# Optimization experiments

Hardware: AMD Instinct MI355X
Metric: run time of the kernel (lower is better)

## Reference

```python
import jax, jax.numpy as jnp
import numpy as np

L, B, T, D, H, M = 2, 4, 1024, 256, 4, 1024
EPS = 1e-5  # hk.LayerNorm default


def setup_inputs() -> dict:
    key = jax.random.key(0)
    ks = jax.random.split(key, 12)
    s_in = (2.0 / D) ** 0.5       # VarianceScaling(2.0), fan_in = D
    s_o = (2.0 / (H * D)) ** 0.5  # fan_in = H*D for final projection
    s_m = (1.0 / M) ** 0.5
    g = lambda k, shape, s: jax.random.normal(k, shape, jnp.float32) * s
    return {
        "queries": g(ks[0], (B, T, D), 1.0),
        "Wq": g(ks[1], (L, D, H * D), s_in),
        "bq": jnp.zeros((L, H * D), jnp.float32),
        "Wk": g(ks[2], (L, D, H * D), s_in),
        "bk": jnp.zeros((L, H * D), jnp.float32),
        "Wv": g(ks[3], (L, D, H * D), s_in),
        "bv": jnp.zeros((L, H * D), jnp.float32),
        "Wo": g(ks[4], (L, H * D, D), s_o),
        "bo": jnp.zeros((L, D), jnp.float32),
        "ln1_s": jnp.ones((L, D), jnp.float32),
        "ln1_b": jnp.zeros((L, D), jnp.float32),
        "W1": g(ks[5], (L, D, M), s_in),
        "b1": jnp.zeros((L, M), jnp.float32),
        "W2": g(ks[6], (L, M, D), s_m),
        "b2": jnp.zeros((L, D), jnp.float32),
        "ln2_s": jnp.ones((L, D), jnp.float32),
        "ln2_b": jnp.zeros((L, D), jnp.float32),
    }


def _layernorm(x, s, o):
    m = jnp.mean(x, axis=-1, keepdims=True)
    v = jnp.var(x, axis=-1, keepdims=True)
    return (x - m) * jax.lax.rsqrt(v + EPS) * s + o


def _block(x, Wq, bq, Wk, bk, Wv, bv, Wo, bo, ln1_s, ln1_b, W1, b1, W2, b2, ln2_s, ln2_b):
    # Multi-head self-attention with per-head dim = D (key_size == qkv_size)
    q = (x @ Wq + bq).reshape(B, T, H, D)
    k = (x @ Wk + bk).reshape(B, T, H, D)
    v = (x @ Wv + bv).reshape(B, T, H, D)
    q = q / jnp.sqrt(jnp.float32(D))
    attn = jnp.einsum('bqhd,bkhd->bhqk', q, k)   # [B,H,T,T]
    attn = jax.nn.softmax(attn, axis=-1)
    o = jnp.einsum('bhqk,bkhd->bqhd', attn, v).reshape(B, T, H * D)
    o = o @ Wo + bo
    # post-norm residual 1
    x = _layernorm(o + x, ln1_s, ln1_b)
    # MLP: Linear(D->M) + ReLU + Linear(M->D)
    h = jax.nn.relu(x @ W1 + b1)
    m = h @ W2 + b2
    return _layernorm(m + x, ln2_s, ln2_b)


def reference(queries, Wq, bq, Wk, bk, Wv, bv, Wo, bo, ln1_s, ln1_b,
              W1, b1, W2, b2, ln2_s, ln2_b):
    x = queries
    for i in range(L):
        x = _block(x, Wq[i], bq[i], Wk[i], bk[i], Wv[i], bv[i], Wo[i], bo[i],
                   ln1_s[i], ln1_b[i], W1[i], b1[i], W2[i], b2[i],
                   ln2_s[i], ln2_b[i])
    return x
```

## Files before the change

### kernel.cpp

```cpp
#include <hip/hip_runtime.h>
#include <hip/hip_bf16.h>

#define CL 2
#define CB 4
#define CT 1024
#define CD 256
#define CH 4
#define CM 1024
#define CHD (CH * CD)
#define NROW (CB * CT)

typedef unsigned short ushort_t;
typedef __attribute__((ext_vector_type(8))) short short8v;
typedef __attribute__((ext_vector_type(4))) float float4v;

#define LOG2E 1.44269504088896f

__device__ __forceinline__ float bf2f(unsigned short u) {
    return __uint_as_float(((unsigned int)u) << 16);
}
__device__ __forceinline__ unsigned short f2bf(float f) {
    unsigned int x = __float_as_uint(f);
    return (unsigned short)((x + 0x7fffu + ((x >> 16) & 1u)) >> 16);
}

__global__ __launch_bounds__(256) void detect_kernel(
    const ushort_t* __restrict__ w, int n, int* __restrict__ flag)
{
    __shared__ int red[256];
    int c = 0;
    for (int i = threadIdx.x; i < n; i += 256) {
        float v = bf2f(w[i]);
        if (!(fabsf(v) <= 1e6f)) c++;
    }
    red[threadIdx.x] = c;
    __syncthreads();
    for (int s = 128; s > 0; s >>= 1) {
        if (threadIdx.x < s) red[threadIdx.x] += red[threadIdx.x + s];
        __syncthreads();
    }
    if (threadIdx.x == 0) flag[0] = (red[0] < 8) ? 1 : 0;
}

__global__ __launch_bounds__(256) void tconv_all(
    const void* __restrict__ Wq, const void* __restrict__ Wk,
    const void* __restrict__ Wv, const void* __restrict__ W1,
    ushort_t* __restrict__ wqkvT, ushort_t* __restrict__ w1T,
    const int* __restrict__ flagp)
{
    const int fbf = *flagp;
    const int z = blockIdx.z;
    const int which = z >> 1, l = z & 1;
    const void* in = (which == 0) ? Wq : (which == 1) ? Wk
                   : (which == 2) ? Wv : W1;
    ushort_t* out = (which < 3)
        ? wqkvT + (long)l * 3072 * 256 + (long)which * 1024 * 256
        : w1T + (long)l * 1024 * 256;
    const long zi = (long)l * 262144;

    __shared__ float tile[32][33];
    const int r0 = blockIdx.y * 32;
    const int c0 = blockIdx.x * 32;
    const int tx = threadIdx.x & 31;
    const int ty = threadIdx.x >> 5;
#pragma unroll
    for (int i = 0; i < 32; i += 8) {
        const long idx = zi + (long)(r0 + ty + i) * 1024 + c0 + tx;
        tile[ty + i][tx] = fbf ? bf2f(((const ushort_t*)in)[idx])
                               : ((const float*)in)[idx];
    }
    __syncthreads();
#pragma unroll
    for (int i = 0; i < 32; i += 8)
        out[(long)(c0 + ty + i) * 256 + r0 + tx] = f2bf(tile[tx][ty + i]);
}

__global__ __launch_bounds__(256) void qkv_tconv(
    const ushort_t* __restrict__ A, const ushort_t* __restrict__ B,
    const void* __restrict__ bq, const void* __restrict__ bk,
    const void* __restrict__ bv, ushort_t* __restrict__ qk,
    ushort_t* __restrict__ vT,
    const void* __restrict__ Wo, const void* __restrict__ W2,
    ushort_t* __restrict__ wscr,
    long boff, long ioff, const int* __restrict__ flagp)
{
    __shared__ __align__(16) ushort_t As[128 * 40];
    __shared__ __align__(16) ushort_t Bs[128 * 40];
    __shared__ float tile[32][33];

    const int fbf = *flagp;
    const int bx = blockIdx.x;
    const int tid = threadIdx.x;

    if (bx >= 768) {
        const int t = bx - 768;
        const int zx = t & 7;
        const int zy = (t >> 3) & 31;
        const int zz = t >> 8;
        const void* in = zz ? W2 : Wo;
        ushort_t* out = wscr + (long)zz * 262144;
        const int r0 = zy * 32;
        const int c0 = zx * 32;
        const int tx = tid & 31;
        const int ty = tid >> 5;
#pragma unroll
        for (int i = 0; i < 32; i += 8) {
            const long idx = ioff + (long)(r0 + ty + i) * 256 + c0 + tx;
            tile[ty + i][tx] = fbf ? bf2f(((const ushort_t*)in)[idx])
                                   : ((const float*)in)[idx];
        }
        __syncthreads();
#pragma unroll
        for (int i = 0; i < 32; i += 8)
            out[(long)(c0 + ty + i) * 1024 + r0 + tx] = f2bf(tile[tx][ty + i]);
        return;
    }

    const int nt = bx % 24;
    const int mt = bx / 24;
    const long m0 = (long)mt * 128;
    const long n0 = (long)nt * 128;

    const int wave = tid >> 6;
    const int lane = tid & 63;
    const int quad = lane >> 4;
    const int lrow = lane & 15;
    const int wm = (wave >> 1) * 64;
    const int wn = (wave & 1) * 64;

    float4v acc[4][4];
#pragma unroll
    for (int i = 0; i < 4; ++i)
#pragma unroll
        for (int j = 0; j < 4; ++j)
            acc[i][j] = (float4v){0.f, 0.f, 0.f, 0.f};

    for (int k0 = 0; k0 < 256; k0 += 32) {
        __syncthreads();
#pragma unroll
        for (int p = 0; p < 2; ++p) {
            const int c = p * 256 + tid;
            const int row = c >> 2;
            const int kk = (c & 3) << 3;
            *reinterpret_cast<short8v*>(&As[row * 40 + kk]) =
                *reinterpret_cast<const short8v*>(&A[(m0 + row) * 256 + k0 + kk]);
            *reinterpret_cast<short8v*>(&Bs[row * 40 + kk]) =
                *reinterpret_cast<const short8v*>(&B[(n0 + row) * 256 + k0 + kk]);
        }
        __syncthreads();

        short8v af[4], bfv[4];
#pragma unroll
        for (int i = 0; i < 4; ++i) {
            af[i]  = *reinterpret_cast<const short8v*>(&As[(wm + i * 16 + lrow) * 40 + quad * 8]);
            bfv[i] = *reinterpret_cast<const short8v*>(&Bs[(wn + i * 16 + lrow) * 40 + quad * 8]);
        }
#pragma unroll
        for (int mi = 0; mi < 4; ++mi)
#pragma unroll
            for (int ni = 0; ni < 4; ++ni)
                acc[mi][ni] = __builtin_amdgcn_mfma_f32_16x16x32_bf16(
                    af[mi], bfv[ni], acc[mi][ni], 0, 0, 0);
    }

#pragma unroll
    for (int mi = 0; mi < 4; ++mi) {
#pragma unroll
        for (int ni = 0; ni < 4; ++ni) {
            const long col = n0 + wn + ni * 16 + lrow;
            const long row0 = m0 + wm + mi * 16 + quad * 4;
            const void* bp;
            long bn;
            if (col < 1024)      { bp = bq; bn = col; }
            else if (col < 2048) { bp = bk; bn = col - 1024; }
            else                 { bp = bv; bn = col - 2048; }
            const float bias = fbf ? bf2f(((const ushort_t*)bp)[boff + bn])
                                   : ((const float*)bp)[boff + bn];
            if (col < 2048) {
#pragma unroll
                for (int r = 0; r < 4; ++r)
                    qk[(row0 + r) * 2048 + col] = f2bf(acc[mi][ni][r] + bias);
            } else {
                const long d = col - 2048;
                const long addr = ((row0 >> 10) << 2) * 262144 + d * 1024 + (row0 & 1023);
                ushort4 u;
                u.x = f2bf(acc[mi][ni][0] + bias);
                u.y = f2bf(acc[mi][ni][1] + bias);
                u.z = f2bf(acc[mi][ni][2] + bias);
                u.w = f2bf(acc[mi][ni][3] + bias);
                *reinterpret_cast<ushort4*>(&vT[addr]) = u;
            }
        }
    }
}

template <int AMODE>
__global__ __launch_bounds__(256) void mgemm64s(
    const ushort_t* __restrict__ A, const ushort_t* __restrict__ Ap1,
    const float2* __restrict__ ml, const ushort_t* __restrict__ B,
    float* __restrict__ P, int K2, int lda, int ldb)
{
    const int z = blockIdx.z;
    const long m0 = (long)blockIdx.y * 64;
    const long n0 = (long)blockIdx.x * 64;
    const int k_beg = z * K2;

    __shared__ __align__(16) ushort_t As[64 * 72];
    __shared__ __align__(16) ushort_t Bs[64 * 72];

    const int tid = threadIdx.x;
    const int wave = tid >> 6;
    const int lane = tid & 63;
    const int quad = lane >> 4;
    const int lrow = lane & 15;
    const int wm = (wave >> 1) * 32;
    const int wn = (wave & 1) * 32;

    const int ar = tid >> 2;
    const int ak = (tid & 3) << 3;

    float s0h[2] = {0.f, 0.f}, s1h[2] = {0.f, 0.f};
    if constexpr (AMODE == 1) {
        const long m = m0 + ar;
        const int bhbase = ((int)(m >> 10) << 2);
        const int trow = (int)(m & 1023);
        const int h0 = k_beg >> 8;
#pragma unroll
        for (int i = 0; i < 2; ++i) {
            const int bh = bhbase + h0 + i;
            const float2 v0 = ml[bh * 1024 + trow];
            const float2 v1 = ml[(16 + bh) * 1024 + trow];
            const float mm = fmaxf(v0.x, v1.x);
            const float a0 = exp2f(v0.x - mm);
            const float a1 = exp2f(v1.x - mm);
            const float inv = 1.0f / (v0.y * a0 + v1.y * a1);
            s0h[i] = a0 * inv;
            s1h[i] = a1 * inv;
        }
    }

    float4v acc[2][2];
#pragma unroll
    for (int i = 0; i < 2; ++i)
#pragma unroll
        for (int j = 0; j < 2; ++j)
            acc[i][j] = (float4v){0.f, 0.f, 0.f, 0.f};

    for (int k0 = k_beg; k0 < k_beg + K2; k0 += 64) {
        __syncthreads();
#pragma unroll
        for (int p = 0; p < 2; ++p) {
            const int kc = p * 32 + ak;
            if constexpr (AMODE == 0) {
                *reinterpret_cast<short8v*>(&As[ar * 72 + kc]) =
                    *reinterpret_cast<const short8v*>(&A[(m0 + ar) * (long)lda + k0 + kc]);
            } else {
                const long m = m0 + ar;
                const int hi = ((k0 + kc) >> 8) - (k_beg >> 8);
                const float s0 = s0h[hi], s1 = s1h[hi];
                const ushort4 u0a = *reinterpret_cast<const ushort4*>(&A[m * 1024 + k0 + kc]);
                const ushort4 u0b = *reinterpret_cast<const ushort4*>(&A[m * 1024 + k0 + kc + 4]);
                const ushort4 u1a = *reinterpret_cast<const ushort4*>(&Ap1[m * 1024 + k0 + kc]);
                const ushort4 u1b = *reinterpret_cast<const ushort4*>(&Ap1[m * 1024 + k0 + kc + 4]);
                short8v t8;
                t8[0] = (short)f2bf(bf2f(u0a.x) * s0 + bf2f(u1a.x) * s1);
                t8[1] = (short)f2bf(bf2f(u0a.y) * s0 + bf2f(u1a.y) * s1);
                t8[2] = (short)f2bf(bf2f(u0a.z) * s0 + bf2f(u1a.z) * s1);
                t8[3] = (short)f2bf(bf2f(u0a.w) * s0 + bf2f(u1a.w) * s1);
                t8[4] = (short)f2bf(bf2f(u0b.x) * s0 + bf2f(u1b.x) * s1);
                t8[5] = (short)f2bf(bf2f(u0b.y) * s0 + bf2f(u1b.y) * s1);
                t8[6] = (short)f2bf(bf2f(u0b.z) * s0 + bf2f(u1b.z) * s1);
                t8[7] = (short)f2bf(bf2f(u0b.w) * s0 + bf2f(u1b.w) * s1);
                *reinterpret_cast<short8v*>(&As[ar * 72 + kc]) = t8;
            }
            *reinterpret_cast<short8v*>(&Bs[ar * 72 + kc]) =
                *reinterpret_cast<const short8v*>(&B[(n0 + ar) * (long)ldb + k0 + kc]);
        }
        __syncthreads();

#pragma unroll
        for (int kk = 0; kk < 2; ++kk) {
            short8v af[2], bfv[2];
#pragma unroll
            for (int i = 0; i < 2; ++i) {
                af[i]  = *reinterpret_cast<const short8v*>(
                    &As[(wm + i * 16 + lrow) * 72 + kk * 32 + quad * 8]);
                bfv[i] = *reinterpret_cast<const short8v*>(
                    &Bs[(wn + i * 16 + lrow) * 72 + kk * 32 + quad * 8]);
            }
#pragma unroll
            for (int mi = 0; mi < 2; ++mi)
#pragma unroll
                for (int ni = 0; ni < 2; ++ni)
                    acc[mi][ni] = __builtin_amdgcn_mfma_f32_16x16x32_bf16(
                        af[mi], bfv[ni], acc[mi][ni], 0, 0, 0);
        }
    }

    float* Pz = P + (long)z * NROW * CD;
#pragma unroll
    for (int mi = 0; mi < 2; ++mi)
#pragma unroll
        for (int ni = 0; ni < 2; ++ni) {
            const long col = n0 + wn + ni * 16 + lrow;
            const long row0 = m0 + wm + mi * 16 + quad * 4;
#pragma unroll
            for (int r = 0; r < 4; ++r)
                Pz[(row0 + r) * CD + col] = acc[mi][ni][r];
        }
}

template <int RELU>
__global__ __launch_bounds__(256) void mgemm64b(
    const ushort_t* __restrict__ A, const ushort_t* __restrict__ B,
    const void* __restrict__ bias, ushort_t* __restrict__ C,
    int K, int lda, int ldb, int ldc, long boff,
    const int* __restrict__ flagp)
{
    const long m0 = (long)blockIdx.y * 64;
    const long n0 = (long)blockIdx.x * 64;

    __shared__ __align__(16) ushort_t As[64 * 72];
    __shared__ __align__(16) ushort_t Bs[64 * 72];

    const int tid = threadIdx.x;
    const int wave = tid >> 6;
    const int lane = tid & 63;
    const int quad = lane >> 4;
    const int lrow = lane & 15;
    const int wm = (wave >> 1) * 32;
    const int wn = (wave & 1) * 32;

    const int ar = tid >> 2;
    const int ak = (tid & 3) << 3;

    float4v acc[2][2];
#pragma unroll
    for (int i = 0; i < 2; ++i)
#pragma unroll
        for (int j = 0; j < 2; ++j)
            acc[i][j] = (float4v){0.f, 0.f, 0.f, 0.f};

    for (int k0 = 0; k0 < K; k0 += 64) {
        __syncthreads();
#pragma unroll
        for (int p = 0; p < 2; ++p) {
            const int kc = p * 32 + ak;
            *reinterpret_cast<short8v*>(&As[ar * 72 + kc]) =
                *reinterpret_cast<const short8v*>(&A[(m0 + ar) * (long)lda + k0 + kc]);
            *reinterpret_cast<short8v*>(&Bs[ar * 72 + kc]) =
                *reinterpret_cast<const short8v*>(&B[(n0 + ar) * (long)ldb + k0 + kc]);
        }
        __syncthreads();

#pragma unroll
        for (int kk = 0; kk < 2; ++kk) {
            short8v af[2], bfv[2];
#pragma unroll
            for (int i = 0; i < 2; ++i) {
                af[i]  = *reinterpret_cast<const short8v*>(
                    &As[(wm + i * 16 + lrow) * 72 + kk * 32 + quad * 8]);
                bfv[i] = *reinterpret_cast<const short8v*>(
                    &Bs[(wn + i * 16 + lrow) * 72 + kk * 32 + quad * 8]);
            }
#pragma unroll
            for (int mi = 0; mi < 2; ++mi)
#pragma unroll
                for (int ni = 0; ni < 2; ++ni)
                    acc[mi][ni] = __builtin_amdgcn_mfma_f32_16x16x32_bf16(
                        af[mi], bfv[ni], acc[mi][ni], 0, 0, 0);
        }
    }

    const int fbf = *flagp;
#pragma unroll
    for (int mi = 0; mi < 2; ++mi)
#pragma unroll
        for (int ni = 0; ni < 2; ++ni) {
            const long col = n0 + wn + ni * 16 + lrow;
            const long row0 = m0 + wm + mi * 16 + quad * 4;
            const float bv = fbf ? bf2f(((const ushort_t*)bias)[boff + col])
                                 : ((const float*)bias)[boff + col];
#pragma unroll
            for (int r = 0; r < 4; ++r) {
                float v = acc[mi][ni][r] + bv;
                if (RELU) v = fmaxf(v, 0.f);
                C[(row0 + r) * (long)ldc + col] = f2bf(v);
            }
        }
}

__global__ __launch_bounds__(256) void flash_attn(
    const ushort_t* __restrict__ qk, const ushort_t* __restrict__ vT,
    ushort_t* __restrict__ op0, ushort_t* __restrict__ op1,
    float2* __restrict__ ml)
{
    const int bx = blockIdx.x;
    const int bh = bx & 15;
    const int qt = (bx >> 4) & 15;
    const int ck = bx >> 8;
    const int b = bh >> 2, h = bh & 3;

    __shared__ __align__(16) ushort_t Ks[32 * 264];
    __shared__ __align__(16) ushort_t Vs[256 * 40];
    __shared__ __align__(16) ushort_t Ps[4][16 * 40];

    const int tid = threadIdx.x;
    const int wave = tid >> 6;
    const int lane = tid & 63;
    const int quad = lane >> 4;
    const int lrow = lane & 15;

    const long qrow0 = (long)b * CT + qt * 64;
    const int qcol = h * 256;
    const int kcol = 1024 + h * 256;
    const long vbase = (long)bh * 256 * 1024;
    const float SC = 0.0625f * LOG2E;

    short8v qf[8];
#pragma unroll
    for (int kk = 0; kk < 8; ++kk)
        qf[kk] = *reinterpret_cast<const short8v*>(
            &qk[(qrow0 + wave * 16 + lrow) * 2048 + qcol + kk * 32 + quad * 8]);

    float mrun = -1e30f, lrun = 0.f;
    float4v oacc[16];
#pragma unroll
    for (int i = 0; i < 16; ++i) oacc[i] = (float4v){0.f, 0.f, 0.f, 0.f};

    const int t_beg = ck * 512;
    for (int t0 = t_beg; t0 < t_beg + 512; t0 += 32) {
        __syncthreads();
#pragma unroll
        for (int p = 0; p < 4; ++p) {
            const int c = p * 256 + tid;
            {
                const int r = c >> 5, col = (c & 31) * 8;
                *reinterpret_cast<short8v*>(&Ks[r * 264 + col]) =
                    *reinterpret_cast<const short8v*>(
                        &qk[((long)b * CT + t0 + r) * 2048 + kcol + col]);
            }
            {
                const int r = c >> 2, col = (c & 3) * 8;
                *reinterpret_cast<short8v*>(&Vs[r * 40 + col]) =
                    *reinterpret_cast<const short8v*>(
                        &vT[vbase + (long)r * 1024 + t0 + col]);
            }
        }
        __syncthreads();

        float4v sacc[2];
        sacc[0] = (float4v){0.f, 0.f, 0.f, 0.f};
        sacc[1] = (float4v){0.f, 0.f, 0.f, 0.f};
#pragma unroll
        for (int kk = 0; kk < 8; ++kk) {
#pragma unroll
            for (int ni = 0; ni < 2; ++ni) {
                short8v bk = *reinterpret_cast<const short8v*>(
                    &Ks[(ni * 16 + lrow) * 264 + kk * 32 + quad * 8]);
                sacc[ni] = __builtin_amdgcn_mfma_f32_16x16x32_bf16(
                    bk, qf[kk], sacc[ni], 0, 0, 0);
            }
        }
#pragma unroll
        for (int ni = 0; ni < 2; ++ni)
#pragma unroll
            for (int r = 0; r < 4; ++r)
                sacc[ni][r] *= SC;

        float mx = fmaxf(fmaxf(fmaxf(sacc[0][0], sacc[0][1]),
                               fmaxf(sacc[0][2], sacc[0][3])),
                         fmaxf(fmaxf(sacc[1][0], sacc[1][1]),
                               fmaxf(sacc[1][2], sacc[1][3])));
        mx = fmaxf(mx, __shfl_xor(mx, 16));
        mx = fmaxf(mx, __shfl_xor(mx, 32));

        if (__ballot(mx > mrun + 1.0f) != 0ull) {
            const float mnew = fmaxf(mrun, mx);
            const float alpha = exp2f(mrun - mnew);
            mrun = mnew;
            lrun *= alpha;
            float a4[4];
#pragma unroll
            for (int r = 0; r < 4; ++r)
                a4[r] = __shfl(alpha, quad * 4 + r);
#pragma unroll
            for (int ni = 0; ni < 16; ++ni)
#pragma unroll
                for (int r = 0; r < 4; ++r)
                    oacc[ni][r] *= a4[r];
        }

        float s = 0.f;
#pragma unroll
        for (int ni = 0; ni < 2; ++ni) {
            ushort4 pu;
#pragma unroll
            for (int r = 0; r < 4; ++r) {
                const float pv = exp2f(sacc[ni][r] - mrun);
                s += pv;
                (&pu.x)[r] = f2bf(pv);
            }
            *reinterpret_cast<ushort4*>(
                &Ps[wave][lrow * 40 + ni * 16 + quad * 4]) = pu;
        }
        s += __shfl_xor(s, 16);
        s += __shfl_xor(s, 32);
        lrun += s;

        {
            short8v ap = *reinterpret_cast<const short8v*>(
                &Ps[wave][lrow * 40 + quad * 8]);
#pragma unroll
            for (int ni = 0; ni < 16; ++ni) {
                short8v bv = *reinterpret_cast<const short8v*>(
                    &Vs[(ni * 16 + lrow) * 40 + quad * 8]);
                oacc[ni] = __builtin_amdgcn_mfma_f32_16x16x32_bf16(
                    ap, bv, oacc[ni], 0, 0, 0);
            }
        }
    }

    if (quad == 0)
        ml[((ck << 4) + bh) * 1024 + qt * 64 + wave * 16 + lrow] =
            make_float2(mrun, lrun);

    ushort_t* op = ck ? op1 : op0;
#pragma unroll
    for (int ni = 0; ni < 16; ++ni)
#pragma unroll
        for (int r = 0; r < 4; ++r)
            op[(qrow0 + wave * 16 + quad * 4 + r) * 1024 + (h << 8) + ni * 16 + lrow]
                = f2bf(oacc[ni][r]);
}

template <int FINAL>
__global__ __launch_bounds__(256) void ln_p(
    const float* __restrict__ p, const void* __restrict__ gb, long gboff,
    const ushort_t* __restrict__ res, const void* __restrict__ sc,
    const void* __restrict__ bi, void* __restrict__ out, long loff,
    const int* __restrict__ flagp)
{
    const int fbf = *flagp;
    const long row = (long)blockIdx.x * CD;
    const int t = threadIdx.x;
    const float gbv = fbf ? bf2f(((const ushort_t*)gb)[gboff + t])
                          : ((const float*)gb)[gboff + t];
    const float x = p[row + t] + p[(long)NROW * CD + row + t] + gbv + bf2f(res[row + t]);

    __shared__ float r1[256];
    __shared__ float r2[256];
    r1[t] = x;
    r2[t] = x * x;
    __syncthreads();
    for (int s = 128; s > 0; s >>= 1) {
        if (t < s) { r1[t] += r1[t + s]; r2[t] += r2[t + s]; }
        __syncthreads();
    }
    const float mean = r1[0] * (1.0f / CD);
    const float var = r2[0] * (1.0f / CD) - mean * mean;
    const float rstd = rsqrtf(var + 1e-5f);
    const float s_v = fbf ? bf2f(((const ushort_t*)sc)[loff + t]) : ((const float*)sc)[loff + t];
    const float b_v = fbf ? bf2f(((const ushort_t*)bi)[loff + t]) : ((const float*)bi)[loff + t];
    const float y = (x - mean) * rstd * s_v + b_v;
    if constexpr (FINAL) {
        if (fbf) ((ushort_t*)out)[row + t] = f2bf(y);
        else     ((float*)out)[row + t] = y;
    } else {
        ((ushort_t*)out)[row + t] = f2bf(y);
    }
}

__global__ __launch_bounds__(256) void in_convert(
    const void* __restrict__ in, ushort_t* __restrict__ x,
    const int* __restrict__ flagp)
{
    const int fbf = *flagp;
    const long i = ((long)blockIdx.x * 256 + threadIdx.x) << 2;
    if (fbf) {
        *reinterpret_cast<ushort4*>(x + i) =
            *reinterpret_cast<const ushort4*>((const ushort_t*)in + i);
    } else {
        float4 f = *reinterpret_cast<const float4*>((const float*)in + i);
        ushort4 u;
        u.x = f2bf(f.x); u.y = f2bf(f.y); u.z = f2bf(f.z); u.w = f2bf(f.w);
        *reinterpret_cast<ushort4*>(x + i) = u;
    }
}

extern "C" void kernel_launch(void* const* d_in, const int* in_sizes, int n_in,
                              void* d_out, int out_size, void* d_ws, size_t ws_size,
                              hipStream_t stream)
{
    const void* queries = d_in[0];
    const void* Wq = d_in[1];  const void* bq = d_in[2];
    const void* Wk = d_in[3];  const void* bk = d_in[4];
    const void* Wv = d_in[5];  const void* bv = d_in[6];
    const void* Wo = d_in[7];  const void* bo = d_in[8];
    const void* ln1s = d_in[9];  const void* ln1b = d_in[10];
    const void* W1 = d_in[11]; const void* b1 = d_in[12];
    const void* W2 = d_in[13]; const void* b2 = d_in[14];
    const void* ln2s = d_in[15]; const void* ln2b = d_in[16];

    char* p = (char*)d_ws;
    int* flagp = (int*)p;             p += 256;
    ushort_t* wqkvT = (ushort_t*)p;   p += (long)CL * 3072 * 256 * 2;
    ushort_t* w1T   = (ushort_t*)p;   p += (long)CL * 1024 * 256 * 2;
    ushort_t* wscr  = (ushort_t*)p;   p += (long)2 * 256 * 1024 * 2;
    ushort_t* xa    = (ushort_t*)p;   p += (long)NROW * CD * 2;
    ushort_t* qk    = (ushort_t*)p;   p += (long)NROW * 2048 * 2;
    ushort_t* vT    = (ushort_t*)p;   p += (long)16 * 256 * 1024 * 2;
    ushort_t* op0   = (ushort_t*)p;   p += (long)NROW * 1024 * 2;
    ushort_t* op1   = (ushort_t*)p;   p += (long)NROW * 1024 * 2;
    float2*   ml    = (float2*)p;     p += (long)2 * 16 * 1024 * 8;
    ushort_t* h     = vT;
    float*    pgem  = (float*)qk;

    detect_kernel<<<1, 256, 0, stream>>>((const ushort_t*)Wq, 2048, flagp);
    tconv_all<<<dim3(32, 8, 8), 256, 0, stream>>>(
        Wq, Wk, Wv, W1, wqkvT, w1T, flagp);
    in_convert<<<(NROW * CD) / 1024, 256, 0, stream>>>(queries, xa, flagp);

    for (int l = 0; l < CL; ++l) {
        qkv_tconv<<<dim3(1280, 1, 1), 256, 0, stream>>>(
            xa, wqkvT + (long)l * 3072 * 256, bq, bk, bv, qk, vT,
            Wo, W2, wscr, (long)l * 1024, (long)l * 1024 * 256, flagp);
        flash_attn<<<512, 256, 0, stream>>>(qk, vT, op0, op1, ml);
        mgemm64s<1><<<dim3(4, 64, 2), 256, 0, stream>>>(
            op0, op1, ml, wscr, pgem, 512, 1024, 1024);
        ln_p<0><<<NROW, 256, 0, stream>>>(pgem, bo, (long)l * 256, xa,
                                          ln1s, ln1b, xa, (long)l * 256, flagp);
        mgemm64b<1><<<dim3(16, 64, 1), 256, 0, stream>>>(
            xa, w1T + (long)l * 1024 * 256, b1, h,
            256, 256, 256, 1024, (long)l * 1024, flagp);
        mgemm64s<0><<<dim3(4, 64, 2), 256, 0, stream>>>(
            h, nullptr, nullptr, wscr + 262144, pgem, 512, 1024, 1024);
        if (l == CL - 1)
            ln_p<1><<<NROW, 256, 0, stream>>>(pgem, b2, (long)l * 256, xa,
                                              ln2s, ln2b, d_out, (long)l * 256, flagp);
        else
            ln_p<0><<<NROW, 256, 0, stream>>>(pgem, b2, (long)l * 256, xa,
                                              ln2s, ln2b, xa, (long)l * 256, flagp);
    }
}
```

Before: 304.2 us.

## Double-buffer K/V tiles in flash attention with register prefetch and MFMA priority

Flash attention now prefetches the next K and V tile into registers while the current tile is computed, and stores it into alternating shared-memory buffers. This drops one barrier per iteration and lets global loads overlap MFMA work. Raised wave priority (s_setprio) is also placed around the MFMA loops. In exchange the kernel uses twice the LDS for K/V and 8 extra vector registers per thread, which may reduce occupancy.

```diff
diff --git a/kernel.cpp b/kernel.cpp
--- a/kernel.cpp
+++ b/kernel.cpp
@@ -401,8 +401,8 @@
     const int ck = bx >> 8;
     const int b = bh >> 2, h = bh & 3;
 
-    __shared__ __align__(16) ushort_t Ks[32 * 264];
-    __shared__ __align__(16) ushort_t Vs[256 * 40];
+    __shared__ __align__(16) ushort_t Ks[2][32 * 264];
+    __shared__ __align__(16) ushort_t Vs[2][256 * 40];
     __shared__ __align__(16) ushort_t Ps[4][16 * 40];
 
     const int tid = threadIdx.x;
@@ -428,40 +428,60 @@
 #pragma unroll
     for (int i = 0; i < 16; ++i) oacc[i] = (float4v){0.f, 0.f, 0.f, 0.f};
 
+    const int krow_b = tid >> 5;
+    const int kcol8  = (tid & 31) * 8;
+    const int vrow_b = tid >> 2;
+    const int vcol8  = (tid & 3) * 8;
+
+    short8v kreg[4], vreg[4];
+
     const int t_beg = ck * 512;
+
+#pragma unroll
+    for (int p = 0; p < 4; ++p) {
+        kreg[p] = *reinterpret_cast<const short8v*>(
+            &qk[((long)b * CT + t_beg + p * 8 + krow_b) * 2048 + kcol + kcol8]);
+        vreg[p] = *reinterpret_cast<const short8v*>(
+            &vT[vbase + (long)(p * 64 + vrow_b) * 1024 + t_beg + vcol8]);
+    }
+
     for (int t0 = t_beg; t0 < t_beg + 512; t0 += 32) {
-        __syncthreads();
+        const int bsel = (t0 >> 5) & 1;
+
 #pragma unroll
         for (int p = 0; p < 4; ++p) {
-            const int c = p * 256 + tid;
-            {
-                const int r = c >> 5, col = (c & 31) * 8;
-                *reinterpret_cast<short8v*>(&Ks[r * 264 + col]) =
-                    *reinterpret_cast<const short8v*>(
-                        &qk[((long)b * CT + t0 + r) * 2048 + kcol + col]);
-            }
-            {
-                const int r = c >> 2, col = (c & 3) * 8;
-                *reinterpret_cast<short8v*>(&Vs[r * 40 + col]) =
-                    *reinterpret_cast<const short8v*>(
-                        &vT[vbase + (long)r * 1024 + t0 + col]);
-            }
-        }
+            *reinterpret_cast<short8v*>(&Ks[bsel][(p * 8 + krow_b) * 264 + kcol8]) = kreg[p];
+            *reinterpret_cast<short8v*>(&Vs[bsel][(p * 64 + vrow_b) * 40 + vcol8]) = vreg[p];
+        }
+
+        if (t0 + 32 < t_beg + 512) {
+            const int tn = t0 + 32;
+#pragma unroll
+            for (int p = 0; p < 4; ++p) {
+                kreg[p] = *reinterpret_cast<const short8v*>(
+                    &qk[((long)b * CT + tn + p * 8 + krow_b) * 2048 + kcol + kcol8]);
+                vreg[p] = *reinterpret_cast<const short8v*>(
+                    &vT[vbase + (long)(p * 64 + vrow_b) * 1024 + tn + vcol8]);
+            }
+        }
+
         __syncthreads();
 
         float4v sacc[2];
         sacc[0] = (float4v){0.f, 0.f, 0.f, 0.f};
         sacc[1] = (float4v){0.f, 0.f, 0.f, 0.f};
+        __builtin_amdgcn_s_setprio(1);
 #pragma unroll
         for (int kk = 0; kk < 8; ++kk) {
 #pragma unroll
             for (int ni = 0; ni < 2; ++ni) {
                 short8v bk = *reinterpret_cast<const short8v*>(
-                    &Ks[(ni * 16 + lrow) * 264 + kk * 32 + quad * 8]);
+                    &Ks[bsel][(ni * 16 + lrow) * 264 + kk * 32 + quad * 8]);
                 sacc[ni] = __builtin_amdgcn_mfma_f32_16x16x32_bf16(
                     bk, qf[kk], sacc[ni], 0, 0, 0);
             }
         }
+        __builtin_amdgcn_s_setprio(0);
 #pragma unroll
         for (int ni = 0; ni < 2; ++ni)
 #pragma unroll
@@ -511,13 +531,15 @@
         {
             short8v ap = *reinterpret_cast<const short8v*>(
                 &Ps[wave][lrow * 40 + quad * 8]);
+            __builtin_amdgcn_s_setprio(1);
 #pragma unroll
             for (int ni = 0; ni < 16; ++ni) {
                 short8v bv = *reinterpret_cast<const short8v*>(
-                    &Vs[(ni * 16 + lrow) * 40 + quad * 8]);
+                    &Vs[bsel][(ni * 16 + lrow) * 40 + quad * 8]);
                 oacc[ni] = __builtin_amdgcn_mfma_f32_16x16x32_bf16(
                     ap, bv, oacc[ni], 0, 0, 0);
             }
+            __builtin_amdgcn_s_setprio(0);
         }
     }
 
```

Result: no change. 301.3 us (median of 2 runs) (-0.9%).

## Rewrite flash attention with 32x32 MFMA, register P, and double-buffered K/V

Applied to the files above, without the earlier changes.

Restructures the flash attention kernel so each wave owns 32 query rows and uses 32x32x16 bf16 MFMAs, which halves the block count to 256. The P matrix is now passed between lanes by shuffles instead of going through shared memory. K and V tiles are double-buffered in LDS and prefetched through registers, with an XOR swizzle on K to avoid bank conflicts, so there is one barrier per iteration instead of two. The cost is higher register pressure and fewer blocks, which may leave part of the 256 CUs idle.

```diff
diff --git a/kernel.cpp b/kernel.cpp
--- a/kernel.cpp
+++ b/kernel.cpp
@@ -13,6 +13,7 @@
 typedef unsigned short ushort_t;
 typedef __attribute__((ext_vector_type(8))) short short8v;
 typedef __attribute__((ext_vector_type(4))) float float4v;
+typedef __attribute__((ext_vector_type(16))) float float16v;
 
 #define LOG2E 1.44269504088896f
 
@@ -390,89 +391,108 @@
         }
 }
 
-__global__ __launch_bounds__(256) void flash_attn(
+__global__ __launch_bounds__(256, 1) void flash_attn(
     const ushort_t* __restrict__ qk, const ushort_t* __restrict__ vT,
     ushort_t* __restrict__ op0, ushort_t* __restrict__ op1,
     float2* __restrict__ ml)
 {
     const int bx = blockIdx.x;
     const int bh = bx & 15;
-    const int qt = (bx >> 4) & 15;
-    const int ck = bx >> 8;
-    const int b = bh >> 2, h = bh & 3;
-
-    __shared__ __align__(16) ushort_t Ks[32 * 264];
-    __shared__ __align__(16) ushort_t Vs[256 * 40];
-    __shared__ __align__(16) ushort_t Ps[4][16 * 40];
+    const int qg = (bx >> 4) & 7;
+    const int ck = bx >> 7;
+    const int bb = bh >> 2, h = bh & 3;
+
+    __shared__ __align__(16) ushort_t Ks[2][32 * 256];
+    __shared__ __align__(16) ushort_t Vs[2][256 * 40];
 
     const int tid = threadIdx.x;
     const int wave = tid >> 6;
     const int lane = tid & 63;
-    const int quad = lane >> 4;
-    const int lrow = lane & 15;
-
-    const long qrow0 = (long)b * CT + qt * 64;
+    const int col = lane & 31;
+    const int hi = lane >> 5;
+    const int hi8 = hi << 3;
+
+    const long qrow0w = (long)bb * CT + qg * 128 + wave * 32;
     const int qcol = h * 256;
     const int kcol = 1024 + h * 256;
     const long vbase = (long)bh * 256 * 1024;
     const float SC = 0.0625f * LOG2E;
-
-    short8v qf[8];
-#pragma unroll
-    for (int kk = 0; kk < 8; ++kk)
-        qf[kk] = *reinterpret_cast<const short8v*>(
-            &qk[(qrow0 + wave * 16 + lrow) * 2048 + qcol + kk * 32 + quad * 8]);
+    const int t_beg = ck * 512;
+
+    const int kr_ = tid >> 5;
+    const int kc_ = (tid & 31) << 3;
+    const int vr_ = tid >> 2;
+    const int vc_ = (tid & 3) << 3;
+
+    short8v kreg[4], vreg[4];
+#pragma unroll
+    for (int i = 0; i < 4; ++i) {
+        kreg[i] = *reinterpret_cast<const short8v*>(
+            &qk[((long)bb * CT + t_beg + i * 8 + kr_) * 2048 + kcol + kc_]);
+        vreg[i] = *reinterpret_cast<const short8v*>(
+            &vT[vbase + (long)(i * 64 + vr_) * 1024 + t_beg + vc_]);
+    }
+
+    short8v qf[16];
+#pragma unroll
+    for (int s = 0; s < 16; ++s)
+        qf[s] = *reinterpret_cast<const short8v*>(
+            &qk[(qrow0w + col) * 2048 + qcol + s * 16 + hi8]);
 
     float mrun = -1e30f, lrun = 0.f;
-    float4v oacc[16];
-#pragma unroll
-    for (int i = 0; i < 16; ++i) oacc[i] = (float4v){0.f, 0.f, 0.f, 0.f};
-
-    const int t_beg = ck * 512;
-    for (int t0 = t_beg; t0 < t_beg + 512; t0 += 32) {
-        __syncthreads();
-#pragma unroll
-        for (int p = 0; p < 4; ++p) {
-            const int c = p * 256 + tid;
-            {
-                const int r = c >> 5, col = (c & 31) * 8;
-                *reinterpret_cast<short8v*>(&Ks[r * 264 + col]) =
-                    *reinterpret_cast<const short8v*>(
-                        &qk[((long)b * CT + t0 + r) * 2048 + kcol + col]);
+    float16v oacc[8];
+#pragma unroll
+    for (int i = 0; i < 8; ++i)
+#pragma unroll
+        for (int j = 0; j < 16; ++j) oacc[i][j] = 0.f;
+
+#pragma unroll
+    for (int i = 0; i < 4; ++i) {
+        const int kr = i * 8 + kr_;
+        *reinterpret_cast<short8v*>(
+            &Ks[0][kr * 256 + (((tid & 31) ^ kr) << 3)]) = kreg[i];
+        *reinterpret_cast<short8v*>(
+            &Vs[0][(i * 64 + vr_) * 40 + vc_]) = vreg[i];
+    }
+    __syncthreads();
+
+    const int krowbase = col * 256;
+    const int kxor = col << 4;
+
+    for (int it = 0; it < 16; ++it) {
+        const int cur = it & 1;
+
+        if (it < 15) {
+            const int tn = t_beg + (it + 1) * 32;
+#pragma unroll
+            for (int i = 0; i < 4; ++i) {
+                kreg[i] = *reinterpret_cast<const short8v*>(
+                    &qk[((long)bb * CT + tn + i * 8 + kr_) * 2048 + kcol + kc_]);
+                vreg[i] = *reinterpret_cast<const short8v*>(
+                    &vT[vbase + (long)(i * 64 + vr_) * 1024 + tn + vc_]);
             }
-            {
-                const int r = c >> 2, col = (c & 3) * 8;
-                *reinterpret_cast<short8v*>(&Vs[r * 40 + col]) =
-                    *reinterpret_cast<const short8v*>(
-                        &vT[vbase + (long)r * 1024 + t0 + col]);
-            }
-        }
-        __syncthreads();
-
-        float4v sacc[2];
-        sacc[0] = (float4v){0.f, 0.f, 0.f, 0.f};
-        sacc[1] = (float4v){0.f, 0.f, 0.f, 0.f};
-#pragma unroll
-        for (int kk = 0; kk < 8; ++kk) {
-#pragma unroll
-            for (int ni = 0; ni < 2; ++ni) {
-                short8v bk = *reinterpret_cast<const short8v*>(
-                    &Ks[(ni * 16 + lrow) * 264 + kk * 32 + quad * 8]);
-                sacc[ni] = __builtin_amdgcn_mfma_f32_16x16x32_bf16(
-                    bk, qf[kk], sacc[ni], 0, 0, 0);
-            }
-        }
-#pragma unroll
-        for (int ni = 0; ni < 2; ++ni)
-#pragma unroll
-            for (int r = 0; r < 4; ++r)
-                sacc[ni][r] *= SC;
-
-        float mx = fmaxf(fmaxf(fmaxf(sacc[0][0], sacc[0][1]),
-                               fmaxf(sacc[0][2], sacc[0][3])),
-                         fmaxf(fmaxf(sacc[1][0], sacc[1][1]),
-                               fmaxf(sacc[1][2], sacc[1][3])));
-        mx = fmaxf(mx, __shfl_xor(mx, 16));
+        }
+
+        float16v sa, sb;
+#pragma unroll
+        for (int j = 0; j < 16; ++j) { sa[j] = 0.f; sb[j] = 0.f; }
+#pragma unroll
+        for (int s = 0; s < 16; s += 2) {
+            const int o0 = ((s * 32 + hi * 16) ^ kxor) >> 1;
+            const int o1 = (((s + 1) * 32 + hi * 16) ^ kxor) >> 1;
+            const short8v k0 = *reinterpret_cast<const short8v*>(&Ks[cur][krowbase + o0]);
+            const short8v k1 = *reinterpret_cast<const short8v*>(&Ks[cur][krowbase + o1]);
+            sa = __builtin_amdgcn_mfma_f32_32x32x16_bf16(k0, qf[s], sa, 0, 0, 0);
+            sb = __builtin_amdgcn_mfma_f32_32x32x16_bf16(k1, qf[s + 1], sb, 0, 0, 0);
+        }
+
+        float sv[16];
+#pragma unroll
+        for (int j = 0; j < 16; ++j) sv[j] = (sa[j] + sb[j]) * SC;
+
+        float mx = sv[0];
+#pragma unroll
+        for (int j = 1; j < 16; ++j) mx = fmaxf(mx, sv[j]);
         mx = fmaxf(mx, __shfl_xor(mx, 32));
 
         if (__ballot(mx > mrun + 1.0f) != 0ull) {
@@ -480,58 +500,85 @@
             const float alpha = exp2f(mrun - mnew);
             mrun = mnew;
             lrun *= alpha;
-            float a4[4];
-#pragma unroll
-            for (int r = 0; r < 4; ++r)
-                a4[r] = __shfl(alpha, quad * 4 + r);
-#pragma unroll
-            for (int ni = 0; ni < 16; ++ni)
-#pragma unroll
-                for (int r = 0; r < 4; ++r)
-                    oacc[ni][r] *= a4[r];
-        }
-
+            float ar[16];
+#pragma unroll
+            for (int r = 0; r < 16; ++r)
+                ar[r] = __shfl(alpha, (r & 3) + 8 * (r >> 2) + (hi << 2));
+#pragma unroll
+            for (int dt = 0; dt < 8; ++dt)
+#pragma unroll
+                for (int r = 0; r < 16; ++r)
+                    oacc[dt][r] *= ar[r];
+        }
+
+        float p[16];
         float s = 0.f;
 #pragma unroll
-        for (int ni = 0; ni < 2; ++ni) {
-            ushort4 pu;
-#pragma unroll
-            for (int r = 0; r < 4; ++r) {
-                const float pv = exp2f(sacc[ni][r] - mrun);
-                s += pv;
-                (&pu.x)[r] = f2bf(pv);
-            }
-            *reinterpret_cast<ushort4*>(
-                &Ps[wave][lrow * 40 + ni * 16 + quad * 4]) = pu;
-        }
-        s += __shfl_xor(s, 16);
+        for (int j = 0; j < 16; ++j) { p[j] = exp2f(sv[j] - mrun); s += p[j]; }
         s += __shfl_xor(s, 32);
         lrun += s;
 
-        {
-            short8v ap = *reinterpret_cast<const short8v*>(
-                &Ps[wave][lrow * 40 + quad * 8]);
-#pragma unroll
-            for (int ni = 0; ni < 16; ++ni) {
-                short8v bv = *reinterpret_cast<const short8v*>(
-                    &Vs[(ni * 16 + lrow) * 40 + quad * 8]);
-                oacc[ni] = __builtin_amdgcn_mfma_f32_16x16x32_bf16(
-                    ap, bv, oacc[ni], 0, 0, 0);
+        const unsigned c01 = (unsigned)f2bf(p[0])  | ((unsigned)f2bf(p[1])  << 16);
+        const unsigned c23 = (unsigned)f2bf(p[2])  | ((unsigned)f2bf(p[3])  << 16);
+        const unsigned c45 = (unsigned)f2bf(p[4])  | ((unsigned)f2bf(p[5])  << 16);
+        const unsigned c67 = (unsigned)f2bf(p[6])  | ((unsigned)f2bf(p[7])  << 16);
+        const unsigned d01 = (unsigned)f2bf(p[8])  | ((unsigned)f2bf(p[9])  << 16);
+        const unsigned d23 = (unsigned)f2bf(p[10]) | ((unsigned)f2bf(p[11]) << 16);
+        const unsigned d45 = (unsigned)f2bf(p[12]) | ((unsigned)f2bf(p[13]) << 16);
+        const unsigned d67 = (unsigned)f2bf(p[14]) | ((unsigned)f2bf(p[15]) << 16);
+        const unsigned x01 = __shfl_xor(c01, 32);
+        const unsigned x23 = __shfl_xor(c23, 32);
+        const unsigned x45 = __shfl_xor(c45, 32);
+        const unsigned x67 = __shfl_xor(c67, 32);
+        const unsigned y01 = __shfl_xor(d01, 32);
+        const unsigned y23 = __shfl_xor(d23, 32);
+        const unsigned y45 = __shfl_xor(d45, 32);
+        const unsigned y67 = __shfl_xor(d67, 32);
+        union { unsigned u[4]; short8v v; } pf0, pf1;
+        pf0.u[0] = hi ? x45 : c01;
+        pf0.u[1] = hi ? x67 : c23;
+        pf0.u[2] = hi ? c45 : x01;
+        pf0.u[3] = hi ? c67 : x23;
+        pf1.u[0] = hi ? y45 : d01;
+        pf1.u[1] = hi ? y67 : d23;
+        pf1.u[2] = hi ? d45 : y01;
+        pf1.u[3] = hi ? d67 : y23;
+
+#pragma unroll
+        for (int dt = 0; dt < 8; ++dt) {
+            const int vb = (dt * 32 + col) * 40 + hi8;
+            const short8v v0 = *reinterpret_cast<const short8v*>(&Vs[cur][vb]);
+            const short8v v1 = *reinterpret_cast<const short8v*>(&Vs[cur][vb + 16]);
+            oacc[dt] = __builtin_amdgcn_mfma_f32_32x32x16_bf16(pf0.v, v0, oacc[dt], 0, 0, 0);
+            oacc[dt] = __builtin_amdgcn_mfma_f32_32x32x16_bf16(pf1.v, v1, oacc[dt], 0, 0, 0);
+        }
+
+        if (it < 15) {
+            const int nb = cur ^ 1;
+#pragma unroll
+            for (int i = 0; i < 4; ++i) {
+                const int kr = i * 8 + kr_;
+                *reinterpret_cast<short8v*>(
+                    &Ks[nb][kr * 256 + (((tid & 31) ^ kr) << 3)]) = kreg[i];
+                *reinterpret_cast<short8v*>(
+                    &Vs[nb][(i * 64 + vr_) * 40 + vc_]) = vreg[i];
             }
-        }
-    }
-
-    if (quad == 0)
-        ml[((ck << 4) + bh) * 1024 + qt * 64 + wave * 16 + lrow] =
-            make_float2(mrun, lrun);
-
+            __syncthreads();
+        }
+    }
+
+    if (lane < 32) {
+        const int trow = (int)((qrow0w + lane) & 1023);
+        ml[((ck << 4) + bh) * 1024 + trow] = make_float2(mrun, lrun);
+    }
     ushort_t* op = ck ? op1 : op0;
 #pragma unroll
-    for (int ni = 0; ni < 16; ++ni)
-#pragma unroll
-        for (int r = 0; r < 4; ++r)
-            op[(qrow0 + wave * 16 + quad * 4 + r) * 1024 + (h << 8) + ni * 16 + lrow]
-                = f2bf(oacc[ni][r]);
+    for (int dt = 0; dt < 8; ++dt)
+#pragma unroll
+        for (int r = 0; r < 16; ++r) {
+            const int row = (r & 3) + 8 * (r >> 2) + (hi << 2);
+            op[(qrow0w + row) * 1024 + (h << 8) + dt * 32 + col] = f2bf(oacc[dt][r]);
+        }
 }
 
 template <int FINAL>
@@ -625,7 +672,7 @@
         qkv_tconv<<<dim3(1280, 1, 1), 256, 0, stream>>>(
             xa, wqkvT + (long)l * 3072 * 256, bq, bk, bv, qk, vT,
             Wo, W2, wscr, (long)l * 1024, (long)l * 1024 * 256, flagp);
-        flash_attn<<<512, 256, 0, stream>>>(qk, vT, op0, op1, ml);
+        flash_attn<<<256, 256, 0, stream>>>(qk, vT, op0, op1, ml);
         mgemm64s<1><<<dim3(4, 64, 2), 256, 0, stream>>>(
             op0, op1, ml, wscr, pgem, 512, 1024, 1024);
         ln_p<0><<<NROW, 256, 0, stream>>>(pgem, bo, (long)l * 256, xa,
```

New measurement: 316.5 us. +4.0%, slower.
